# Optimization experiments

Hardware: AMD Instinct MI355X
Metric: run time of the kernel (lower is better)

Reference implementation:

```python
import jax, jax.numpy as jnp
import numpy as np

LORA_RANK = 16
LORA_ALPHA = 32
CHUNK_SIZE = 256
TTT_LR = 0.01
CLIP_THRESHOLD = 1.0
SCALING = LORA_ALPHA / LORA_RANK
LN_EPS = 1e-5


def setup_inputs() -> dict:
    key = jax.random.key(0)
    ks = jax.random.split(key, 5)
    B, S, K, H = 2, 8192, 1024, 1024
    x = jax.random.normal(ks[0], (B, S, K), dtype=jnp.float32)
    Wb = jax.random.normal(ks[1], (H, K), dtype=jnp.float32) / np.sqrt(K)
    init_A = jax.random.normal(ks[2], (H, LORA_RANK), dtype=jnp.float32) * 0.01
    init_B = jax.random.normal(ks[3], (LORA_RANK, K), dtype=jnp.float32) * 0.01
    ln_gamma = jnp.ones((K,), dtype=jnp.float32)
    ln_beta = jnp.zeros((K,), dtype=jnp.float32)
    Wp = jax.random.normal(ks[4], (H, K), dtype=jnp.float32) / np.sqrt(K)
    return {"x": x, "Wb": Wb, "init_A": init_A, "init_B": init_B,
            "ln_gamma": ln_gamma, "ln_beta": ln_beta, "Wp": Wp}


def _forward(x, Wb, init_A, init_B, ln_gamma, ln_beta, Wp):
    B_sz, Seq, k_dim = x.shape
    h_dim = Wb.shape[0]
    r = init_A.shape[1]
    nc = Seq // CHUNK_SIZE  # Seq chosen divisible; pad_len == 0

    base_out = x @ Wb.T  # [B, S, H]

    # --- target construction under no_grad: LayerNorm + left-shift ---
    xd = jax.lax.stop_gradient(x)
    mu = jnp.mean(xd, axis=-1, keepdims=True)
    var = jnp.mean((xd - mu) ** 2, axis=-1, keepdims=True)
    xn = (xd - mu) * jax.lax.rsqrt(var + LN_EPS) * ln_gamma + ln_beta
    shifted = jnp.pad(xn[:, 1:, :], ((0, 0), (0, 1), (0, 0)))
    shifted = jax.lax.stop_gradient(shifted)

    V = shifted @ Wp.T  # [B, S, H]

    Z = x.reshape(B_sz * nc, CHUNK_SIZE, k_dim)
    Vc = V.reshape(B_sz * nc, CHUNK_SIZE, h_dim)

    # per-chunk fast-weight deltas
    proj_in = Z @ init_B.T                                # [BC, C, r]
    dA = jnp.einsum('bch,bcr->bhr', Vc, proj_in)          # [BC, H, r]
    proj_err = Vc @ init_A                                # [BC, C, r]
    dB = jnp.einsum('bcr,bck->brk', proj_err, Z)          # [BC, r, K]

    dA = dA.reshape(B_sz, nc, h_dim, r)
    dB = dB.reshape(B_sz, nc, r, k_dim)

    # exclusive cross-chunk cumsum
    accA = jnp.cumsum(dA, axis=1)
    accB = jnp.cumsum(dB, axis=1)
    accA = jnp.concatenate([jnp.zeros_like(accA[:, :1]), accA[:, :-1]], axis=1)
    accB = jnp.concatenate([jnp.zeros_like(accB[:, :1]), accB[:, :-1]], axis=1)

    lr = TTT_LR * SCALING
    rawA = (lr * accA).reshape(-1, h_dim, r)
    rawB = (lr * accB).reshape(-1, r, k_dim)

    # joint norm clip (norm_type=2)
    norm_sq = (jnp.sum(rawA.astype(jnp.float32) ** 2, axis=(-2, -1), keepdims=True)
               + jnp.sum(rawB.astype(jnp.float32) ** 2, axis=(-2, -1), keepdims=True))
    total_norm = jnp.sqrt(norm_sq)
    coef = jnp.minimum(CLIP_THRESHOLD / (total_norm + 1e-6), 1.0).astype(rawA.dtype)

    A_eff = init_A[None] - rawA * coef  # [BC, H, r]
    B_eff = init_B[None] - rawB * coef  # [BC, r, K]

    mid = jnp.einsum('bck,brk->bcr', Z, B_eff)          # [BC, C, r]
    lora = jnp.einsum('bcr,bhr->bch', mid, A_eff)       # [BC, C, H]
    lora = lora.reshape(B_sz, Seq, h_dim)

    return base_out + lora * SCALING


def reference(x, Wb, init_A, init_B, ln_gamma, ln_beta, Wp):
    return _forward(x, Wb, init_A, init_B, ln_gamma, ln_beta, Wp)
```

## Files before the change

kernel.cpp:

```cpp
#include <hip/hip_runtime.h>

typedef __attribute__((ext_vector_type(8))) short s16x8;
typedef __attribute__((ext_vector_type(4))) float f32x4;
typedef unsigned short u16;

#define B_SZ 2
#define SEQ 8192
#define KD 1024
#define HD 1024
#define RK 16
#define CH 256
#define NCH 64
static constexpr float LR_SC = 0.02f;
static constexpr float SCALE_OUT = 2.0f;

__device__ __forceinline__ u16 f2b(float f) {
  union { float f; unsigned int u; } c; c.f = f;
  unsigned int u = c.u;
  unsigned int r = (u + 0x7fffu + ((u >> 16) & 1u)) >> 16;
  return (u16)r;
}
__device__ __forceinline__ float b2f(u16 v) {
  union { unsigned int u; float f; } c; c.u = ((unsigned int)v) << 16; return c.f;
}
__device__ __forceinline__ void async16(const u16* g, u16* l) {
  __builtin_amdgcn_global_load_lds((const __attribute__((address_space(1))) void*)g,
                                   (__attribute__((address_space(3))) void*)l, 16, 0, 0);
}

__global__ __launch_bounds__(256) void cvt_bf16(const float* __restrict__ src,
                                                u16* __restrict__ dst, int n) {
  int i = (blockIdx.x * 256 + threadIdx.x) * 4;
  if (i < n) {
    float4 v = *(const float4*)(src + i);
    ushort4 o; o.x = f2b(v.x); o.y = f2b(v.y); o.z = f2b(v.z); o.w = f2b(v.w);
    *(ushort4*)(dst + i) = o;
  }
}

__global__ __launch_bounds__(256) void wpat_part(const float* __restrict__ initA,
                                                 const float* __restrict__ Wp,
                                                 float* __restrict__ part) {
  int t = threadIdx.x;
  int k = blockIdx.x * 256 + t;
  int hseg = blockIdx.y;
  __shared__ float Asm[256 * 16];
  for (int i = t; i < 1024; i += 256)
    *(float4*)&Asm[i * 4] = *(const float4*)&initA[(size_t)hseg * 4096 + i * 4];
  __syncthreads();
  float acc[16];
  #pragma unroll
  for (int j = 0; j < 16; j++) acc[j] = 0.f;
  const float* wp = Wp + (size_t)hseg * 256 * KD + k;
  #pragma unroll 4
  for (int hh = 0; hh < 256; hh++) {
    float w = wp[(size_t)hh * KD];
    const float4* ar = (const float4*)&Asm[hh * 16];
    #pragma unroll
    for (int q = 0; q < 4; q++) {
      float4 a = ar[q];
      acc[q*4+0] += w * a.x; acc[q*4+1] += w * a.y;
      acc[q*4+2] += w * a.z; acc[q*4+3] += w * a.w;
    }
  }
  float* o = part + ((size_t)hseg * 1024 + k) * 16;
  #pragma unroll
  for (int q = 0; q < 4; q++) {
    float4 r; r.x = acc[q*4]; r.y = acc[q*4+1]; r.z = acc[q*4+2]; r.w = acc[q*4+3];
    *(float4*)&o[q * 4] = r;
  }
}

__global__ __launch_bounds__(256) void wpat_reduce(const float* __restrict__ part,
                                                   u16* __restrict__ WpAT) {
  int idx = blockIdx.x * 256 + threadIdx.x;
  int k = idx & 1023, r = idx >> 10;
  float s = part[((size_t)0 * 1024 + k) * 16 + r]
          + part[((size_t)1 * 1024 + k) * 16 + r]
          + part[((size_t)2 * 1024 + k) * 16 + r]
          + part[((size_t)3 * 1024 + k) * 16 + r];
  WpAT[(size_t)r * KD + k] = f2b(s);
}

__global__ __launch_bounds__(256) void ln_shift(const float* __restrict__ x,
                                                const float* __restrict__ gamma,
                                                const float* __restrict__ beta,
                                                u16* __restrict__ xb,
                                                u16* __restrict__ shb) {
  int row = blockIdx.x;
  int t = threadIdx.x;
  int s = row & (SEQ - 1);
  const float* xr = x + (size_t)row * KD;
  float4 v = *(const float4*)(xr + t * 4);
  ushort4 o; o.x = f2b(v.x); o.y = f2b(v.y); o.z = f2b(v.z); o.w = f2b(v.w);
  *(ushort4*)(xb + (size_t)row * KD + t * 4) = o;

  if (s == 0) {
    ushort4 z; z.x = 0; z.y = 0; z.z = 0; z.w = 0;
    *(ushort4*)(shb + ((size_t)row + SEQ - 1) * KD + t * 4) = z;
    return;
  }
  float s1 = v.x + v.y + v.z + v.w;
  float s2 = v.x * v.x + v.y * v.y + v.z * v.z + v.w * v.w;
  #pragma unroll
  for (int off = 32; off > 0; off >>= 1) {
    s1 += __shfl_down(s1, off);
    s2 += __shfl_down(s2, off);
  }
  __shared__ float red[8];
  int wave = t >> 6, lane = t & 63;
  if (lane == 0) { red[wave * 2] = s1; red[wave * 2 + 1] = s2; }
  __syncthreads();
  float sum = red[0] + red[2] + red[4] + red[6];
  float ssq = red[1] + red[3] + red[5] + red[7];
  float mu = sum * (1.0f / KD);
  float var = ssq * (1.0f / KD) - mu * mu;
  float rstd = rsqrtf(var + 1e-5f);
  float4 g = *(const float4*)(gamma + t * 4);
  float4 bb = *(const float4*)(beta + t * 4);
  ushort4 so;
  so.x = f2b((v.x - mu) * rstd * g.x + bb.x);
  so.y = f2b((v.y - mu) * rstd * g.y + bb.y);
  so.z = f2b((v.z - mu) * rstd * g.z + bb.z);
  so.w = f2b((v.w - mu) * rstd * g.w + bb.w);
  *(ushort4*)(shb + (size_t)(row - 1) * KD + t * 4) = so;
}

__global__ __launch_bounds__(256, 2) void gemm_fused(const u16* __restrict__ A,
                                                     const u16* __restrict__ Bm,
                                                     const u16* __restrict__ mid2,
                                                     const u16* __restrict__ Aef,
                                                     float* __restrict__ C) {
  constexpr int BM = 128, BN = 128, BK = 32, N = HD, Kd = KD;
  __shared__ u16 As[BM * BK];
  __shared__ u16 Bs[BN * BK];
  int tid = threadIdx.x;
  int lane = tid & 63, wave = tid >> 6;
  int m0 = blockIdx.y * BM, n0 = blockIdx.x * BN;
  int wm = (wave >> 1) * 64, wn = (wave & 1) * 64;
  int lr = lane & 15;
  int swz = (((lane >> 4) ^ ((lr >> 1) & 3)) & 3) * 8;
  f32x4 acc[4][4] = {};

  const u16* gbase; u16* lbase;
  if (wave < 2) { gbase = A + (size_t)(m0 + wave * 64) * Kd; lbase = As + wave * 64 * BK; }
  else          { gbase = Bm + (size_t)(n0 + (wave - 2) * 64) * Kd; lbase = Bs + (wave - 2) * 64 * BK; }
  int srow = lane >> 2;
  int scol = (((lane & 3) ^ ((srow >> 1) & 3)) & 3) * 8;
  const u16* gsrc = gbase + (size_t)srow * Kd + scol;

  for (int k0 = 0; k0 < Kd; k0 += BK) {
    #pragma unroll
    for (int i = 0; i < 4; i++)
      async16(gsrc + (size_t)i * 16 * Kd, lbase + i * 16 * BK);
    gsrc += BK;
    __syncthreads();
    s16x8 af[4], bfr[4];
    #pragma unroll
    for (int i = 0; i < 4; i++) af[i] = *(const s16x8*)(As + (wm + i * 16 + lr) * BK + swz);
    #pragma unroll
    for (int j = 0; j < 4; j++) bfr[j] = *(const s16x8*)(Bs + (wn + j * 16 + lr) * BK + swz);
    #pragma unroll
    for (int i = 0; i < 4; i++)
      #pragma unroll
      for (int j = 0; j < 4; j++)
        acc[i][j] = __builtin_amdgcn_mfma_f32_16x16x32_bf16(af[i], bfr[j], acc[i][j], 0, 0, 0);
    __syncthreads();
  }

  {
    int chunk = blockIdx.y >> 1;
    const u16* abase = Aef + (size_t)chunk * (HD * RK);
    int klane = lane >> 4;
    s16x8 am2[4], bn2[4];
    #pragma unroll
    for (int i = 0; i < 4; i++) {
      if (klane < 2)
        am2[i] = *(const s16x8*)(mid2 + (size_t)(m0 + wm + i * 16 + lr) * RK + klane * 8);
      else { s16x8 z = {}; am2[i] = z; }
    }
    #pragma unroll
    for (int j = 0; j < 4; j++) {
      if (klane < 2)
        bn2[j] = *(const s16x8*)(abase + (size_t)(n0 + wn + j * 16 + lr) * RK + klane * 8);
      else { s16x8 z = {}; bn2[j] = z; }
    }
    #pragma unroll
    for (int i = 0; i < 4; i++)
      #pragma unroll
      for (int j = 0; j < 4; j++)
        acc[i][j] = __builtin_amdgcn_mfma_f32_16x16x32_bf16(am2[i], bn2[j], acc[i][j], 0, 0, 0);
  }

  int rb = (lane >> 4) * 4, cc = lane & 15;
  #pragma unroll
  for (int i = 0; i < 4; i++)
    #pragma unroll
    for (int j = 0; j < 4; j++)
      #pragma unroll
      for (int p = 0; p < 4; p++)
        C[(size_t)(m0 + wm + i * 16 + rb + p) * N + (n0 + wn + j * 16 + cc)] = acc[i][j][p];
}

__global__ __launch_bounds__(256) void rank16_proj(const u16* __restrict__ xb,
                                                   const u16* __restrict__ shb,
                                                   const u16* __restrict__ iBb,
                                                   const u16* __restrict__ WpAT,
                                                   float* __restrict__ pin,
                                                   float* __restrict__ per) {
  const u16* X; const u16* W; float* O;
  if (blockIdx.z == 0) { X = xb; W = iBb; O = pin; }
  else                 { X = shb; W = WpAT; O = per; }
  int wave = threadIdx.x >> 6, lane = threadIdx.x & 63;
  int m0 = (blockIdx.x * 4 + wave) * 16;
  int lr = lane & 15, lk = (lane >> 4) * 8;
  const u16* xp = X + (size_t)(m0 + lr) * KD + lk;
  const u16* wp = W + (size_t)lr * KD + lk;
  f32x4 acc = {};
  #pragma unroll 4
  for (int k0 = 0; k0 < KD; k0 += 32) {
    s16x8 a = *(const s16x8*)xp;
    s16x8 b = *(const s16x8*)wp;
    acc = __builtin_amdgcn_mfma_f32_16x16x32_bf16(a, b, acc, 0, 0, 0);
    xp += 32; wp += 32;
  }
  int rb = (lane >> 4) * 4, cc = lane & 15;
  #pragma unroll
  for (int p = 0; p < 4; p++)
    O[(size_t)(m0 + rb + p) * RK + cc] = acc[p];
}

__global__ __launch_bounds__(256) void rank16_mid(const u16* __restrict__ xb,
                                                  const u16* __restrict__ Bef,
                                                  u16* __restrict__ mid2) {
  int wave = threadIdx.x >> 6, lane = threadIdx.x & 63;
  int m0 = (blockIdx.x * 4 + wave) * 16;
  int chunk = m0 >> 8;
  int lr = lane & 15, lk = (lane >> 4) * 8;
  const u16* xp = xb + (size_t)(m0 + lr) * KD + lk;
  const u16* wp = Bef + (size_t)chunk * (RK * KD) + (size_t)lr * KD + lk;
  f32x4 acc = {};
  #pragma unroll 4
  for (int k0 = 0; k0 < KD; k0 += 32) {
    s16x8 a = *(const s16x8*)xp;
    s16x8 b = *(const s16x8*)wp;
    acc = __builtin_amdgcn_mfma_f32_16x16x32_bf16(a, b, acc, 0, 0, 0);
    xp += 32; wp += 32;
  }
  int rb = (lane >> 4) * 4, cc = lane & 15;
  #pragma unroll
  for (int p = 0; p < 4; p++)
    mid2[(size_t)(m0 + rb + p) * RK + cc] = f2b(SCALE_OUT * acc[p]);
}

__global__ __launch_bounds__(256) void gk_kernel(const u16* __restrict__ xb,
                                                 const u16* __restrict__ shb,
                                                 const float* __restrict__ pin,
                                                 const float* __restrict__ per,
                                                 float* __restrict__ G,
                                                 float* __restrict__ dB) {
  int tile = blockIdx.x;
  int chunk = blockIdx.y;
  int which = blockIdx.z;
  int t = threadIdx.x;
  __shared__ float P[CH * RK];
  const float* psrc = which ? per : pin;
  for (int i = t; i < 1024; i += 256)
    *(float4*)&P[i * 4] = *(const float4*)&psrc[(size_t)chunk * 4096 + i * 4];
  __syncthreads();
  float acc[16];
  #pragma unroll
  for (int j = 0; j < 16; j++) acc[j] = 0.f;
  int col = tile * 256 + t;
  const u16* src = (which ? xb : shb) + (size_t)chunk * CH * KD + col;
  for (int c = 0; c < 256; c++) {
    float v = b2f(src[(size_t)c * 1024]);
    const float4* pr = (const float4*)&P[c * 16];
    #pragma unroll
    for (int q = 0; q < 4; q++) {
      float4 p = pr[q];
      acc[q*4+0] += v * p.x; acc[q*4+1] += v * p.y;
      acc[q*4+2] += v * p.z; acc[q*4+3] += v * p.w;
    }
  }
  float* o = (which ? dB : G) + (size_t)chunk * 16384 + col;
  #pragma unroll
  for (int j = 0; j < 16; j++) o[(size_t)j * 1024] = acc[j];
}

__global__ __launch_bounds__(256) void cumsum_kernel(const float* __restrict__ G,
                                                     const float* __restrict__ dB,
                                                     u16* __restrict__ rawG,
                                                     float* __restrict__ rawB) {
  int idx = blockIdx.x * 256 + threadIdx.x;
  int which = idx >> 15;
  int rem = idx & 32767;
  int b = rem >> 14;
  int e = rem & 16383;
  size_t base = (size_t)b * 32 * 16384 + e;
  if (which == 0) {
    float run = 0.f;
    for (int i = 0; i < 32; i++) {
      size_t off = base + (size_t)i * 16384;
      float nv = G[off];
      rawG[off] = f2b(LR_SC * run);
      run += nv;
    }
  } else {
    float run = 0.f;
    for (int i = 0; i < 32; i++) {
      size_t off = base + (size_t)i * 16384;
      float nv = dB[off];
      rawB[off] = LR_SC * run;
      run += nv;
    }
  }
}

__global__ __launch_bounds__(256) void dagemm(const u16* __restrict__ Wpb,
                                              const u16* __restrict__ rawG,
                                              float* __restrict__ rawA) {
  int wave = threadIdx.x >> 6, lane = threadIdx.x & 63;
  int m0 = (blockIdx.x * 4 + wave) * 16;
  int chunk = blockIdx.y;
  int lr = lane & 15, lk = (lane >> 4) * 8;
  const u16* ap = Wpb + (size_t)(m0 + lr) * KD + lk;
  const u16* bp = rawG + (size_t)chunk * 16384 + (size_t)lr * KD + lk;
  f32x4 acc = {};
  #pragma unroll 4
  for (int k0 = 0; k0 < KD; k0 += 32) {
    s16x8 a = *(const s16x8*)ap;
    s16x8 b = *(const s16x8*)bp;
    acc = __builtin_amdgcn_mfma_f32_16x16x32_bf16(a, b, acc, 0, 0, 0);
    ap += 32; bp += 32;
  }
  int rb = (lane >> 4) * 4, cc = lane & 15;
  #pragma unroll
  for (int p = 0; p < 4; p++)
    rawA[(size_t)chunk * 16384 + (size_t)(m0 + rb + p) * RK + cc] = acc[p];
}

__global__ __launch_bounds__(256) void coef_kernel(const float* __restrict__ rawA,
                                                   const float* __restrict__ rawB,
                                                   float* __restrict__ coef) {
  int chunk = blockIdx.x, t = threadIdx.x;
  const float* a = rawA + (size_t)chunk * 16384;
  const float* b = rawB + (size_t)chunk * 16384;
  float s = 0.f;
  for (int i = t * 4; i < 16384; i += 1024) {
    float4 v = *(const float4*)(a + i);
    s += v.x*v.x + v.y*v.y + v.z*v.z + v.w*v.w;
    float4 w = *(const float4*)(b + i);
    s += w.x*w.x + w.y*w.y + w.z*w.z + w.w*w.w;
  }
  #pragma unroll
  for (int off = 32; off > 0; off >>= 1) s += __shfl_down(s, off);
  __shared__ float red[4];
  int wave = t >> 6, lane = t & 63;
  if (lane == 0) red[wave] = s;
  __syncthreads();
  if (t == 0) {
    float tot = red[0] + red[1] + red[2] + red[3];
    float n = sqrtf(tot);
    coef[chunk] = fminf(1.0f / (n + 1e-6f), 1.0f);
  }
}

__global__ __launch_bounds__(256) void eff_kernel(const float* __restrict__ initA,
                                                  const float* __restrict__ initB,
                                                  const float* __restrict__ rawA,
                                                  const float* __restrict__ rawB,
                                                  const float* __restrict__ coef,
                                                  u16* __restrict__ Aef,
                                                  u16* __restrict__ Bef) {
  int idx = blockIdx.x * 256 + threadIdx.x;
  int which = idx >> 18;
  int rem = idx & 262143;
  int chunk = rem >> 12;
  int e = (rem & 4095) * 4;
  float cf = coef[chunk];
  const float* ini = which ? initB : initA;
  const float* raw = (which ? rawB : rawA) + (size_t)chunk * 16384;
  u16* out = (which ? Bef : Aef) + (size_t)chunk * 16384;
  float4 iv = *(const float4*)(ini + e);
  float4 rv = *(const float4*)(raw + e);
  ushort4 r;
  r.x = f2b(iv.x - rv.x * cf); r.y = f2b(iv.y - rv.y * cf);
  r.z = f2b(iv.z - rv.z * cf); r.w = f2b(iv.w - rv.w * cf);
  *(ushort4*)(out + e) = r;
}

extern "C" void kernel_launch(void* const* d_in, const int* in_sizes, int n_in,
                              void* d_out, int out_size, void* d_ws, size_t ws_size,
                              hipStream_t stream) {
  (void)in_sizes; (void)n_in; (void)out_size; (void)ws_size;
  const float* x     = (const float*)d_in[0];
  const float* Wb    = (const float*)d_in[1];
  const float* initA = (const float*)d_in[2];
  const float* initB = (const float*)d_in[3];
  const float* gamma = (const float*)d_in[4];
  const float* beta  = (const float*)d_in[5];
  const float* Wp    = (const float*)d_in[6];
  float* out = (float*)d_out;

  char* ws = (char*)d_ws;
  size_t off = 0;
  auto alloc = [&](size_t bytes) -> void* {
    void* p = ws + off;
    off = (off + bytes + 255) & ~(size_t)255;
    return p;
  };
  const size_t ROWS = (size_t)B_SZ * SEQ;
  u16* xb    = (u16*)alloc(ROWS * KD * 2);
  u16* shb   = (u16*)alloc(ROWS * KD * 2);
  u16* Wbb   = (u16*)alloc((size_t)HD * KD * 2);
  u16* Wpb   = (u16*)alloc((size_t)HD * KD * 2);
  u16* iBb   = (u16*)alloc((size_t)RK * KD * 2);
  u16* WpAT  = (u16*)alloc((size_t)RK * KD * 2);
  float* wpart = (float*)alloc((size_t)4 * KD * RK * 4);
  float* pin = (float*)alloc((size_t)NCH * CH * RK * 4);
  float* per = (float*)alloc((size_t)NCH * CH * RK * 4);
  float* G   = (float*)alloc((size_t)NCH * 16384 * 4);
  float* dB  = (float*)alloc((size_t)NCH * 16384 * 4);
  u16* rawG  = (u16*)alloc((size_t)NCH * 16384 * 2);
  float* rawB= (float*)alloc((size_t)NCH * 16384 * 4);
  float* rawA= (float*)alloc((size_t)NCH * 16384 * 4);
  float* cf  = (float*)alloc(NCH * 4);
  u16* Aef   = (u16*)alloc((size_t)NCH * 16384 * 2);
  u16* Bef   = (u16*)alloc((size_t)NCH * 16384 * 2);
  u16* mid2  = (u16*)alloc(ROWS * RK * 2);

  cvt_bf16<<<1024, 256, 0, stream>>>(Wb, Wbb, HD * KD);
  cvt_bf16<<<1024, 256, 0, stream>>>(Wp, Wpb, HD * KD);
  cvt_bf16<<<16, 256, 0, stream>>>(initB, iBb, RK * KD);
  wpat_part<<<dim3(4, 4), 256, 0, stream>>>(initA, Wp, wpart);
  wpat_reduce<<<64, 256, 0, stream>>>(wpart, WpAT);
  ln_shift<<<ROWS, 256, 0, stream>>>(x, gamma, beta, xb, shb);
  rank16_proj<<<dim3(256, 1, 2), 256, 0, stream>>>(xb, shb, iBb, WpAT, pin, per);
  gk_kernel<<<dim3(4, NCH, 2), 256, 0, stream>>>(xb, shb, pin, per, G, dB);
  cumsum_kernel<<<256, 256, 0, stream>>>(G, dB, rawG, rawB);
  dagemm<<<dim3(16, NCH), 256, 0, stream>>>(Wpb, rawG, rawA);
  coef_kernel<<<NCH, 256, 0, stream>>>(rawA, rawB, cf);
  eff_kernel<<<2048, 256, 0, stream>>>(initA, initB, rawA, rawB, cf, Aef, Bef);
  rank16_mid<<<256, 256, 0, stream>>>(xb, Bef, mid2);
  gemm_fused<<<dim3(HD / 128, ROWS / 128), 256, 0, stream>>>(xb, Wbb, mid2, Aef, out);
}
```

Baseline: 320.8 us.

## Double GEMM K-tile, remap block order, merge conversion and coef/eff kernels

The main GEMM now loads a 64-wide K tile per iteration, halving the number of barrier-separated loop trips, and uses a new XOR swizzle suited to 8 slots per row. Its block indices are remapped so that consecutive blocks cover scattered M-tiles, which is meant to spread the load across the L2/XCD partitions. The three bf16 conversion launches are merged into one, and the coefficient and effective-weight kernels are fused so the per-chunk coef is computed and applied in the same block. Together these reduce launch overhead and synchronization count, at the cost of doubling LDS use in the GEMM, which may reduce occupancy, and leaving only 64 blocks for the fused eff work.

```diff
diff --git a/kernel.cpp b/kernel.cpp
--- a/kernel.cpp
+++ b/kernel.cpp
@@ -28,14 +28,21 @@
                                    (__attribute__((address_space(3))) void*)l, 16, 0, 0);
 }
 
-__global__ __launch_bounds__(256) void cvt_bf16(const float* __restrict__ src,
-                                                u16* __restrict__ dst, int n) {
-  int i = (blockIdx.x * 256 + threadIdx.x) * 4;
-  if (i < n) {
-    float4 v = *(const float4*)(src + i);
-    ushort4 o; o.x = f2b(v.x); o.y = f2b(v.y); o.z = f2b(v.z); o.w = f2b(v.w);
-    *(ushort4*)(dst + i) = o;
-  }
+__global__ __launch_bounds__(256) void cvt_all(const float* __restrict__ Wb,
+                                               const float* __restrict__ Wp,
+                                               const float* __restrict__ initB,
+                                               u16* __restrict__ Wbb,
+                                               u16* __restrict__ Wpb,
+                                               u16* __restrict__ iBb) {
+  int bid = blockIdx.x;
+  const float* src; u16* dst; int base;
+  if (bid < 1024)      { src = Wb;    dst = Wbb; base = bid; }
+  else if (bid < 2048) { src = Wp;    dst = Wpb; base = bid - 1024; }
+  else                 { src = initB; dst = iBb; base = bid - 2048; }
+  int i = (base * 256 + threadIdx.x) * 4;
+  float4 v = *(const float4*)(src + i);
+  ushort4 o; o.x = f2b(v.x); o.y = f2b(v.y); o.z = f2b(v.z); o.w = f2b(v.w);
+  *(ushort4*)(dst + i) = o;
 }
 
 __global__ __launch_bounds__(256) void wpat_part(const float* __restrict__ initA,
@@ -131,35 +138,51 @@
                                                      const u16* __restrict__ mid2,
                                                      const u16* __restrict__ Aef,
                                                      float* __restrict__ C) {
-  constexpr int BM = 128, BN = 128, BK = 32, N = HD, Kd = KD;
+  constexpr int BM = 128, BN = 128, BK = 64, N = HD, Kd = KD;
   __shared__ u16 As[BM * BK];
   __shared__ u16 Bs[BN * BK];
   int tid = threadIdx.x;
   int lane = tid & 63, wave = tid >> 6;
-  int m0 = blockIdx.y * BM, n0 = blockIdx.x * BN;
+  int lb = blockIdx.x + 8 * blockIdx.y;
+  int q = lb & 7, t = lb >> 3;
+  int mb = q * 16 + (t >> 3);
+  int nb = t & 7;
+  int m0 = mb * 128, n0 = nb * 128;
   int wm = (wave >> 1) * 64, wn = (wave & 1) * 64;
   int lr = lane & 15;
-  int swz = (((lane >> 4) ^ ((lr >> 1) & 3)) & 3) * 8;
+  int qd = lane >> 4;
+  int sw = lr & 7;
+  int slot0 = ((qd ^ sw) * 8);
+  int slot1 = (((4 + qd) ^ sw) * 8);
   f32x4 acc[4][4] = {};
 
   const u16* gbase; u16* lbase;
   if (wave < 2) { gbase = A + (size_t)(m0 + wave * 64) * Kd; lbase = As + wave * 64 * BK; }
   else          { gbase = Bm + (size_t)(n0 + (wave - 2) * 64) * Kd; lbase = Bs + (wave - 2) * 64 * BK; }
-  int srow = lane >> 2;
-  int scol = (((lane & 3) ^ ((srow >> 1) & 3)) & 3) * 8;
+  int srow = lane >> 3;
+  int scol = ((lane & 7) ^ srow) * 8;
   const u16* gsrc = gbase + (size_t)srow * Kd + scol;
 
   for (int k0 = 0; k0 < Kd; k0 += BK) {
     #pragma unroll
-    for (int i = 0; i < 4; i++)
-      async16(gsrc + (size_t)i * 16 * Kd, lbase + i * 16 * BK);
+    for (int i = 0; i < 8; i++)
+      async16(gsrc + (size_t)i * 8 * Kd, lbase + i * 512);
     gsrc += BK;
     __syncthreads();
     s16x8 af[4], bfr[4];
     #pragma unroll
-    for (int i = 0; i < 4; i++) af[i] = *(const s16x8*)(As + (wm + i * 16 + lr) * BK + swz);
-    #pragma unroll
-    for (int j = 0; j < 4; j++) bfr[j] = *(const s16x8*)(Bs + (wn + j * 16 + lr) * BK + swz);
+    for (int i = 0; i < 4; i++) af[i] = *(const s16x8*)(As + (wm + i * 16 + lr) * BK + slot0);
+    #pragma unroll
+    for (int j = 0; j < 4; j++) bfr[j] = *(const s16x8*)(Bs + (wn + j * 16 + lr) * BK + slot0);
+    #pragma unroll
+    for (int i = 0; i < 4; i++)
+      #pragma unroll
+      for (int j = 0; j < 4; j++)
+        acc[i][j] = __builtin_amdgcn_mfma_f32_16x16x32_bf16(af[i], bfr[j], acc[i][j], 0, 0, 0);
+    #pragma unroll
+    for (int i = 0; i < 4; i++) af[i] = *(const s16x8*)(As + (wm + i * 16 + lr) * BK + slot1);
+    #pragma unroll
+    for (int j = 0; j < 4; j++) bfr[j] = *(const s16x8*)(Bs + (wn + j * 16 + lr) * BK + slot1);
     #pragma unroll
     for (int i = 0; i < 4; i++)
       #pragma unroll
@@ -169,7 +192,7 @@
   }
 
   {
-    int chunk = blockIdx.y >> 1;
+    int chunk = m0 >> 8;
     const u16* abase = Aef + (size_t)chunk * (HD * RK);
     int klane = lane >> 4;
     s16x8 am2[4], bn2[4];
@@ -340,9 +363,12 @@
     rawA[(size_t)chunk * 16384 + (size_t)(m0 + rb + p) * RK + cc] = acc[p];
 }
 
-__global__ __launch_bounds__(256) void coef_kernel(const float* __restrict__ rawA,
-                                                   const float* __restrict__ rawB,
-                                                   float* __restrict__ coef) {
+__global__ __launch_bounds__(256) void coef_eff(const float* __restrict__ initA,
+                                                const float* __restrict__ initB,
+                                                const float* __restrict__ rawA,
+                                                const float* __restrict__ rawB,
+                                                u16* __restrict__ Aef,
+                                                u16* __restrict__ Bef) {
   int chunk = blockIdx.x, t = threadIdx.x;
   const float* a = rawA + (size_t)chunk * 16384;
   const float* b = rawB + (size_t)chunk * 16384;
@@ -359,35 +385,24 @@
   int wave = t >> 6, lane = t & 63;
   if (lane == 0) red[wave] = s;
   __syncthreads();
-  if (t == 0) {
-    float tot = red[0] + red[1] + red[2] + red[3];
-    float n = sqrtf(tot);
-    coef[chunk] = fminf(1.0f / (n + 1e-6f), 1.0f);
-  }
-}
-
-__global__ __launch_bounds__(256) void eff_kernel(const float* __restrict__ initA,
-                                                  const float* __restrict__ initB,
-                                                  const float* __restrict__ rawA,
-                                                  const float* __restrict__ rawB,
-                                                  const float* __restrict__ coef,
-                                                  u16* __restrict__ Aef,
-                                                  u16* __restrict__ Bef) {
-  int idx = blockIdx.x * 256 + threadIdx.x;
-  int which = idx >> 18;
-  int rem = idx & 262143;
-  int chunk = rem >> 12;
-  int e = (rem & 4095) * 4;
-  float cf = coef[chunk];
-  const float* ini = which ? initB : initA;
-  const float* raw = (which ? rawB : rawA) + (size_t)chunk * 16384;
-  u16* out = (which ? Bef : Aef) + (size_t)chunk * 16384;
-  float4 iv = *(const float4*)(ini + e);
-  float4 rv = *(const float4*)(raw + e);
-  ushort4 r;
-  r.x = f2b(iv.x - rv.x * cf); r.y = f2b(iv.y - rv.y * cf);
-  r.z = f2b(iv.z - rv.z * cf); r.w = f2b(iv.w - rv.w * cf);
-  *(ushort4*)(out + e) = r;
+  float tot = red[0] + red[1] + red[2] + red[3];
+  float cf = fminf(1.0f / (sqrtf(tot) + 1e-6f), 1.0f);
+  u16* ao = Aef + (size_t)chunk * 16384;
+  u16* bo = Bef + (size_t)chunk * 16384;
+  for (int i = t * 4; i < 16384; i += 1024) {
+    float4 iv = *(const float4*)(initA + i);
+    float4 rv = *(const float4*)(a + i);
+    ushort4 r;
+    r.x = f2b(iv.x - rv.x * cf); r.y = f2b(iv.y - rv.y * cf);
+    r.z = f2b(iv.z - rv.z * cf); r.w = f2b(iv.w - rv.w * cf);
+    *(ushort4*)(ao + i) = r;
+    float4 iw = *(const float4*)(initB + i);
+    float4 rw = *(const float4*)(b + i);
+    ushort4 rr;
+    rr.x = f2b(iw.x - rw.x * cf); rr.y = f2b(iw.y - rw.y * cf);
+    rr.z = f2b(iw.z - rw.z * cf); rr.w = f2b(iw.w - rw.w * cf);
+    *(ushort4*)(bo + i) = rr;
+  }
 }
 
 extern "C" void kernel_launch(void* const* d_in, const int* in_sizes, int n_in,
@@ -425,14 +440,11 @@
   u16* rawG  = (u16*)alloc((size_t)NCH * 16384 * 2);
   float* rawB= (float*)alloc((size_t)NCH * 16384 * 4);
   float* rawA= (float*)alloc((size_t)NCH * 16384 * 4);
-  float* cf  = (float*)alloc(NCH * 4);
   u16* Aef   = (u16*)alloc((size_t)NCH * 16384 * 2);
   u16* Bef   = (u16*)alloc((size_t)NCH * 16384 * 2);
   u16* mid2  = (u16*)alloc(ROWS * RK * 2);
 
-  cvt_bf16<<<1024, 256, 0, stream>>>(Wb, Wbb, HD * KD);
-  cvt_bf16<<<1024, 256, 0, stream>>>(Wp, Wpb, HD * KD);
-  cvt_bf16<<<16, 256, 0, stream>>>(initB, iBb, RK * KD);
+  cvt_all<<<2064, 256, 0, stream>>>(Wb, Wp, initB, Wbb, Wpb, iBb);
   wpat_part<<<dim3(4, 4), 256, 0, stream>>>(initA, Wp, wpart);
   wpat_reduce<<<64, 256, 0, stream>>>(wpart, WpAT);
   ln_shift<<<ROWS, 256, 0, stream>>>(x, gamma, beta, xb, shb);
@@ -440,8 +452,7 @@
   gk_kernel<<<dim3(4, NCH, 2), 256, 0, stream>>>(xb, shb, pin, per, G, dB);
   cumsum_kernel<<<256, 256, 0, stream>>>(G, dB, rawG, rawB);
   dagemm<<<dim3(16, NCH), 256, 0, stream>>>(Wpb, rawG, rawA);
-  coef_kernel<<<NCH, 256, 0, stream>>>(rawA, rawB, cf);
-  eff_kernel<<<2048, 256, 0, stream>>>(initA, initB, rawA, rawB, cf, Aef, Bef);
+  coef_eff<<<NCH, 256, 0, stream>>>(initA, initB, rawA, rawB, Aef, Bef);
   rank16_mid<<<256, 256, 0, stream>>>(xb, Bef, mid2);
-  gemm_fused<<<dim3(HD / 128, ROWS / 128), 256, 0, stream>>>(xb, Wbb, mid2, Aef, out);
-}
+  gemm_fused<<<dim3(8, 128), 256, 0, stream>>>(xb, Wbb, mid2, Aef, out);
+}
```

Result: faster. 314.0 us (-2.1%).
